# Performance work log

Hardware: AMD Instinct MI355X
Metric: run time of the kernel (lower is better)

The kernel has to match this reference:

```python
import jax, jax.numpy as jnp
import numpy as np

N, E = 10000, 80000
IN_C, HID, HEADS = 128, 256, 8
NEG_SLOPE = 0.2


def setup_inputs() -> dict:
    key = jax.random.key(0)
    ks = jax.random.split(key, 16)
    s = lambda k, shape, fan: jax.random.normal(k, shape, jnp.float32) * (1.0 / np.sqrt(fan))
    return {
        "x": jax.random.normal(ks[0], (N, IN_C), jnp.float32),
        "edge_index": jax.random.randint(ks[1], (2, E), 0, N, jnp.int64),
        "edge_weight": jax.random.uniform(ks[2], (E,), jnp.float32),
        # GATConv params
        "W_gat": s(ks[3], (IN_C, HEADS * HID), IN_C),
        "att_src": s(ks[4], (HEADS, HID), HID),
        "att_dst": s(ks[5], (HEADS, HID), HID),
        "b_gat": jnp.zeros((HEADS * HID,), jnp.float32),
        # SAGEConv params (lin_l on aggregated neighbors, lin_r on root)
        "W_sage_l": s(ks[6], (HEADS * HID, HID), HEADS * HID),
        "b_sage_l": jnp.zeros((HID,), jnp.float32),
        "W_sage_r": s(ks[7], (HEADS * HID, HID), HEADS * HID),
        # MLP head
        "W_lin1": s(ks[8], (HID, HID // 2), HID),
        "b_lin1": jnp.zeros((HID // 2,), jnp.float32),
        "W_lin2": s(ks[9], (HID // 2, 1), HID // 2),
        "b_lin2": jnp.zeros((1,), jnp.float32),
    }


def reference(x, edge_index, edge_weight, W_gat, att_src, att_dst, b_gat,
              W_sage_l, b_sage_l, W_sage_r, W_lin1, b_lin1, W_lin2, b_lin2):
    n = x.shape[0]
    src, dst = edge_index[0], edge_index[1]

    # ---- GATConv (edge_attr ignored since edge_dim=None in PyG) ----
    h = (x @ W_gat).reshape(n, HEADS, HID)            # [N,H,C]
    a_src = jnp.sum(h * att_src, axis=-1)             # [N,H]
    a_dst = jnp.sum(h * att_dst, axis=-1)             # [N,H]
    e = a_src[src] + a_dst[dst]                       # [E,H]
    e = jax.nn.leaky_relu(e, NEG_SLOPE)
    # segment softmax over edges sharing a destination node
    e_max = jax.ops.segment_max(e, dst, num_segments=n)   # [N,H]
    e_exp = jnp.exp(e - e_max[dst])                        # [E,H]
    denom = jax.ops.segment_sum(e_exp, dst, num_segments=n)
    alpha = e_exp / (denom[dst] + 1e-16)                   # [E,H]
    msg = h[src] * alpha[:, :, None]                       # [E,H,C]
    out1 = jax.ops.segment_sum(msg, dst, num_segments=n).reshape(n, HEADS * HID) + b_gat
    x1 = jax.nn.relu(out1)                                 # [N, H*C]; dropout is identity at inference

    # ---- SAGEConv (mean aggregation) ----
    deg = jax.ops.segment_sum(jnp.ones((src.shape[0],), x1.dtype), dst, num_segments=n)
    agg = jax.ops.segment_sum(x1[src], dst, num_segments=n) / jnp.maximum(deg, 1.0)[:, None]
    x2 = jax.nn.relu(agg @ W_sage_l + b_sage_l + x1 @ W_sage_r)  # [N, HID]

    # ---- MLP head ----
    hmid = jax.nn.relu(x2 @ W_lin1 + b_lin1)
    return hmid @ W_lin2 + b_lin2                           # [N,1]
```

## Files before the change

### kernel.cpp

```cpp
#include <hip/hip_runtime.h>
#include <math.h>

#define HEADS 8
#define HID 256
#define INC 128
#define GDIM 2048
#define NEG_SLOPE 0.2f
#define KSPLIT 2

typedef unsigned short ushort_t;
typedef short bf16x8 __attribute__((ext_vector_type(8)));
typedef ushort_t u16x8 __attribute__((ext_vector_type(8)));
typedef float f32x4 __attribute__((ext_vector_type(4)));

__device__ __forceinline__ ushort_t f2bf(float f) {
  union { float f; unsigned u; } v; v.f = f;
  unsigned r = (v.u + 0x7FFF + ((v.u >> 16) & 1)) >> 16;
  return (ushort_t)r;
}
__device__ __forceinline__ float bf2f(ushort_t u) {
  union { unsigned u; float f; } v; v.u = ((unsigned)u) << 16;
  return v.f;
}

__device__ __forceinline__ void gload_lds16(const ushort_t* g, ushort_t* l) {
  __builtin_amdgcn_global_load_lds(
      (const __attribute__((address_space(1))) unsigned int*)g,
      (__attribute__((address_space(3))) unsigned int*)l, 16, 0, 0);
}

__device__ __forceinline__ int src_chunk(int lane) {
  return ((lane & 3) - ((lane >> 3) & 3)) & 3;
}
__device__ __forceinline__ int rd_chunk(int lc, int kg) {
  return (kg + ((lc >> 1) & 3)) & 3;
}

__global__ __launch_bounds__(256) void zero_deg(int* __restrict__ deg, int n)
{
  int i = blockIdx.x * 256 + threadIdx.x;
  if (i < n) deg[i] = 0;
}

__global__ __launch_bounds__(256) void prep(
    const float* __restrict__ x, ushort_t* __restrict__ xb,
    const float* __restrict__ Wg, ushort_t* __restrict__ WgT,
    const float* __restrict__ Wl, const float* __restrict__ Wr, ushort_t* __restrict__ WsT,
    const int* __restrict__ ei, int* __restrict__ deg, int E,
    const float* __restrict__ att_s, const float* __restrict__ att_d, float* __restrict__ wt,
    int o1, int o2, int o3, int o4, int o5)
{
  __shared__ float tile[32][33];
  __shared__ float attl[256];
  int b = blockIdx.x, t = threadIdx.x;
  if (b < o1) {
    int i = b * 1024 + t * 4;
    float4 v = *(const float4*)(x + i);
    ushort_t o[4] = {f2bf(v.x), f2bf(v.y), f2bf(v.z), f2bf(v.w)};
    *(unsigned long long*)(xb + i) = *(unsigned long long*)o;
  } else if (b < o4) {
    const float* src; ushort_t* dst; int R, C, rowOff, bx, by;
    if (b < o2)      { int idx = b - o1; src = Wg; dst = WgT; R = INC;  C = GDIM; rowOff = 0;   bx = idx % (INC / 32);  by = idx / (INC / 32); }
    else if (b < o3) { int idx = b - o2; src = Wl; dst = WsT; R = GDIM; C = HID;  rowOff = 0;   bx = idx % (GDIM / 32); by = idx / (GDIM / 32); }
    else             { int idx = b - o3; src = Wr; dst = WsT; R = GDIM; C = HID;  rowOff = HID; bx = idx % (GDIM / 32); by = idx / (GDIM / 32); }
    int tx = t & 31, ty = t >> 5;
    int r0 = bx * 32, c0 = by * 32;
    #pragma unroll
    for (int i = 0; i < 32; i += 8)
      tile[ty + i][tx] = src[(size_t)(r0 + ty + i) * C + c0 + tx];
    __syncthreads();
    #pragma unroll
    for (int i = 0; i < 32; i += 8)
      dst[(size_t)(rowOff + c0 + ty + i) * R + r0 + tx] = f2bf(tile[tx][ty + i]);
  } else if (b < o5) {
    int e = (b - o4) * 256 + t;
    if (e < E) atomicAdd(&deg[ei[E + e]], 1);
  } else {
    int j = b - o5;
    int hd = j & 7;
    const float* att = (j < 8) ? att_s : att_d;
    if (t < 256) attl[t] = att[hd * 256 + t];
    __syncthreads();
    if (t < 128) {
      float acc = 0.f;
      #pragma unroll 8
      for (int c = 0; c < 256; ++c)
        acc += Wg[(size_t)t * GDIM + hd * 256 + c] * attl[c];
      wt[j * 128 + t] = acc;
    }
  }
}

__global__ __launch_bounds__(1024) void scan_deg(const int* __restrict__ deg, int* __restrict__ start,
                                                 int* __restrict__ cursor, int N)
{
  __shared__ int sums[1024];
  int t = threadIdx.x;
  int chunk = (N + 1023) / 1024;
  int s = 0;
  for (int i = 0; i < chunk; ++i) {
    int idx = t * chunk + i;
    if (idx < N) s += deg[idx];
  }
  sums[t] = s;
  __syncthreads();
  for (int off = 1; off < 1024; off <<= 1) {
    int v = (t >= off) ? sums[t - off] : 0;
    __syncthreads();
    sums[t] += v;
    __syncthreads();
  }
  int run = (t == 0) ? 0 : sums[t - 1];
  for (int i = 0; i < chunk; ++i) {
    int idx = t * chunk + i;
    if (idx < N) { start[idx] = run; cursor[idx] = run; run += deg[idx]; }
  }
}

__global__ __launch_bounds__(256) void fill_adots(
    const int* __restrict__ ei, int* __restrict__ cursor, int* __restrict__ srcs, int E, int nbFill,
    const ushort_t* __restrict__ xb, const float* __restrict__ wt,
    float* __restrict__ a_all, int N)
{
  int t = threadIdx.x;
  if (blockIdx.x < nbFill) {
    int e = blockIdx.x * 256 + t;
    if (e < E) {
      int n = ei[E + e];
      int p = atomicAdd(&cursor[n], 1);
      srcs[p] = ei[e];
    }
    return;
  }
  __shared__ float wts[16][132];
  __shared__ ushort_t xs[16 * 128];
  for (int i = t; i < 2048; i += 256) wts[i >> 7][i & 127] = wt[i];
  int b0 = (blockIdx.x - nbFill) * 16;
  {
    int row = t >> 4, off = (t & 15) * 8;
    int n = b0 + row; if (n >= N) n = N - 1;
    *(u16x8*)&xs[row * 128 + off] = *(const u16x8*)(xb + (size_t)n * 128 + off);
  }
  __syncthreads();
  int nl = t >> 4, j = t & 15;
  float acc = 0.f;
  #pragma unroll 8
  for (int k = 0; k < 128; ++k)
    acc += bf2f(xs[nl * 128 + k]) * wts[j][k];
  int n = b0 + nl;
  if (n < N) a_all[(size_t)n * 16 + j] = acc;
}

__global__ __launch_bounds__(256) void gat_aggregate(
    const ushort_t* __restrict__ xb, const float* __restrict__ a_all,
    const int* __restrict__ start, const int* __restrict__ deg,
    const int* __restrict__ srcs, ushort_t* __restrict__ aggb, int N)
{
  int n = blockIdx.x, t = threadIdx.x;
  __shared__ float adst[8];
  __shared__ float emax[8];
  __shared__ float esum[8];
  __shared__ float red[256];
  __shared__ float alpha_s[32][8];
  __shared__ int src_s[32];
  int cnt = deg[n];
  int base = start[n];
  if (t < 8) adst[t] = a_all[(size_t)n * 16 + 8 + t];
  __syncthreads();
  int hd = t & 7, lj = t >> 3;
  float m = -1e30f;
  for (int j = lj; j < cnt; j += 32) {
    int s = srcs[base + j];
    float v = a_all[(size_t)s * 16 + hd] + adst[hd];
    v = v > 0.f ? v : NEG_SLOPE * v;
    m = fmaxf(m, v);
  }
  red[t] = m;
  __syncthreads();
  #pragma unroll
  for (int off = 128; off >= 8; off >>= 1) {
    if (t < off) red[t] = fmaxf(red[t], red[t + off]);
    __syncthreads();
  }
  if (t < 8) emax[t] = red[t];
  __syncthreads();
  float ssum = 0.f;
  for (int j = lj; j < cnt; j += 32) {
    int s = srcs[base + j];
    float v = a_all[(size_t)s * 16 + hd] + adst[hd];
    v = v > 0.f ? v : NEG_SLOPE * v;
    ssum += expf(v - emax[hd]);
  }
  red[t] = ssum;
  __syncthreads();
  #pragma unroll
  for (int off = 128; off >= 8; off >>= 1) {
    if (t < off) red[t] += red[t + off];
    __syncthreads();
  }
  if (t < 8) esum[t] = red[t] + 1e-16f;
  __syncthreads();
  int d = t & 127, hg = t >> 7;
  float acc[4] = {0.f, 0.f, 0.f, 0.f};
  for (int j0 = 0; j0 < cnt; j0 += 32) {
    int j = j0 + lj;
    if (j < cnt) {
      int s = srcs[base + j];
      if (hd == 0) src_s[lj] = s;
      float v = a_all[(size_t)s * 16 + hd] + adst[hd];
      v = v > 0.f ? v : NEG_SLOPE * v;
      alpha_s[lj][hd] = expf(v - emax[hd]) / esum[hd];
    }
    __syncthreads();
    int lim = cnt - j0; if (lim > 32) lim = 32;
    for (int el = 0; el < lim; ++el) {
      float v = bf2f(xb[(size_t)src_s[el] * INC + d]);
      #pragma unroll
      for (int k = 0; k < 4; ++k) acc[k] += v * alpha_s[el][hg * 4 + k];
    }
    __syncthreads();
  }
  #pragma unroll
  for (int k = 0; k < 4; ++k)
    aggb[(size_t)n * 1024 + (hg * 4 + k) * INC + d] = f2bf(acc[k]);
}

__global__ __launch_bounds__(512) void gemm_gat(
    const ushort_t* __restrict__ A, const ushort_t* __restrict__ BT,
    const float* __restrict__ b_gat, ushort_t* __restrict__ x1, int M)
{
  __shared__ ushort_t As[2][128][32];
  __shared__ ushort_t Bs[2][256][32];
  int tid = threadIdx.x;
  int wave = tid >> 6, lane = tid & 63;
  int row0 = blockIdx.x * 128;
  int head = blockIdx.y;
  const ushort_t* Abase = A + head * INC;
  const ushort_t* Bbase = BT + (size_t)head * 256 * INC;
  int wr = (wave >> 2) * 64, wc = (wave & 3) * 64;
  int lc = lane & 15, kg = lane >> 4;
  int sc = src_chunk(lane), srow = lane >> 2;

  f32x4 acc[4][4] = {};

  #define STAGE_G(buf, kt)                                                        \
    {                                                                             \
      int ga = row0 + wave * 16 + srow; if (ga >= M) ga = M - 1;                  \
      gload_lds16(Abase + (size_t)ga * 1024 + (kt) + sc * 8, &As[buf][wave * 16][0]); \
      _Pragma("unroll")                                                           \
      for (int c = 0; c < 2; ++c) {                                               \
        int r = c * 128 + wave * 16 + srow;                                       \
        gload_lds16(Bbase + (size_t)r * INC + (kt) + sc * 8, &Bs[buf][c * 128 + wave * 16][0]); \
      }                                                                           \
    }

  #define COMPUTE_G(buf)                                                          \
    {                                                                             \
      bf16x8 af[4], bfr[4];                                                       \
      _Pragma("unroll")                                                           \
      for (int mi = 0; mi < 4; ++mi)                                              \
        af[mi] = *(const bf16x8*)&As[buf][wr + mi * 16 + lc][rd_chunk(lc, kg) * 8]; \
      _Pragma("unroll")                                                           \
      for (int ni = 0; ni < 4; ++ni)                                              \
        bfr[ni] = *(const bf16x8*)&Bs[buf][wc + ni * 16 + lc][rd_chunk(lc, kg) * 8]; \
      _Pragma("unroll")                                                           \
      for (int mi = 0; mi < 4; ++mi)                                              \
        _Pragma("unroll")                                                         \
        for (int ni = 0; ni < 4; ++ni)                                            \
          acc[mi][ni] = __builtin_amdgcn_mfma_f32_16x16x32_bf16(af[mi], bfr[ni], acc[mi][ni], 0, 0, 0); \
    }

  STAGE_G(0, 0);
  __syncthreads();
  int cur = 0;
  for (int kt = 32; kt < INC; kt += 32) {
    STAGE_G(cur ^ 1, kt);
    COMPUTE_G(cur);
    __syncthreads();
    cur ^= 1;
  }
  COMPUTE_G(cur);
  #undef STAGE_G
  #undef COMPUTE_G

  int gcol0 = head * 256;
  float bg[4];
  #pragma unroll
  for (int ni = 0; ni < 4; ++ni) bg[ni] = b_gat[gcol0 + wc + ni * 16 + lc];
  #pragma unroll
  for (int mi = 0; mi < 4; ++mi) {
    #pragma unroll
    for (int r = 0; r < 4; ++r) {
      int grow = row0 + wr + mi * 16 + kg * 4 + r;
      if (grow < M) {
        #pragma unroll
        for (int ni = 0; ni < 4; ++ni) {
          float v = acc[mi][ni][r] + bg[ni];
          x1[(size_t)grow * GDIM + gcol0 + wc + ni * 16 + lc] = f2bf(v > 0.f ? v : 0.f);
        }
      }
    }
  }
}

__global__ __launch_bounds__(512) void gemm_sage(
    const ushort_t* __restrict__ A, const ushort_t* __restrict__ BT,
    ushort_t* __restrict__ Cp, int M, int Nc, int K, int Klen)
{
  __shared__ ushort_t As[2][128][32];
  __shared__ ushort_t Bs[2][256][32];
  int tid = threadIdx.x;
  int wave = tid >> 6, lane = tid & 63;
  int row0 = blockIdx.x * 128, col0 = blockIdx.y * 256;
  int k0 = blockIdx.z * Klen;
  ushort_t* C = Cp + (size_t)blockIdx.z * M * Nc;
  int wr = (wave >> 2) * 64, wc = (wave & 3) * 64;
  int lc = lane & 15, kg = lane >> 4;
  int sc = src_chunk(lane), srow = lane >> 2;

  f32x4 acc[4][4] = {};

  #define STAGE_S(buf, kt)                                                        \
    {                                                                             \
      int ga = row0 + wave * 16 + srow; if (ga >= M) ga = M - 1;                  \
      gload_lds16(A + (size_t)ga * K + (kt) + sc * 8, &As[buf][wave * 16][0]);    \
      _Pragma("unroll")                                                           \
      for (int c = 0; c < 2; ++c) {                                               \
        int gb = col0 + c * 128 + wave * 16 + srow;                               \
        gload_lds16(BT + (size_t)gb * K + (kt) + sc * 8, &Bs[buf][c * 128 + wave * 16][0]); \
      }                                                                           \
    }

  #define COMPUTE_S(buf)                                                          \
    {                                                                             \
      bf16x8 af[4], bfr[4];                                                       \
      _Pragma("unroll")                                                           \
      for (int mi = 0; mi < 4; ++mi)                                              \
        af[mi] = *(const bf16x8*)&As[buf][wr + mi * 16 + lc][rd_chunk(lc, kg) * 8]; \
      _Pragma("unroll")                                                           \
      for (int ni = 0; ni < 4; ++ni)                                              \
        bfr[ni] = *(const bf16x8*)&Bs[buf][wc + ni * 16 + lc][rd_chunk(lc, kg) * 8]; \
      _Pragma("unroll")                                                           \
      for (int mi = 0; mi < 4; ++mi)                                              \
        _Pragma("unroll")                                                         \
        for (int ni = 0; ni < 4; ++ni)                                            \
          acc[mi][ni] = __builtin_amdgcn_mfma_f32_16x16x32_bf16(af[mi], bfr[ni], acc[mi][ni], 0, 0, 0); \
    }

  STAGE_S(0, k0);
  __syncthreads();
  int cur = 0;
  for (int kt = k0 + 32; kt < k0 + Klen; kt += 32) {
    STAGE_S(cur ^ 1, kt);
    COMPUTE_S(cur);
    __syncthreads();
    cur ^= 1;
  }
  COMPUTE_S(cur);
  #undef STAGE_S
  #undef COMPUTE_S

  #pragma unroll
  for (int mi = 0; mi < 4; ++mi) {
    #pragma unroll
    for (int r = 0; r < 4; ++r) {
      int grow = row0 + wr + mi * 16 + kg * 4 + r;
      if (grow < M) {
        #pragma unroll
        for (int ni = 0; ni < 4; ++ni)
          C[(size_t)grow * Nc + col0 + wc + ni * 16 + lc] = f2bf(acc[mi][ni][r]);
      }
    }
  }
}

__global__ __launch_bounds__(512) void sage_mlp(
    const ushort_t* __restrict__ yp, size_t ypstride,
    const int* __restrict__ start, const int* __restrict__ deg,
    const int* __restrict__ srcs, const float* __restrict__ b_l,
    const float* __restrict__ W1, const float* __restrict__ b1,
    const float* __restrict__ W2, const float* __restrict__ b2, float* __restrict__ out, int N)
{
  __shared__ float xs[16][256];
  __shared__ float wred[8][4];
  const ushort_t* yp0 = yp;
  const ushort_t* yp1 = yp + ypstride;
  int t = threadIdx.x;
  int wv = t >> 6, lane = t & 63;
  int b0 = blockIdx.x * 16;

  int half = lane >> 5;
  int col32 = lane & 31;
  #pragma unroll
  for (int i = 0; i < 2; ++i) {
    int nl = wv * 2 + i;
    int n = b0 + nl;
    float acc[8] = {0.f, 0.f, 0.f, 0.f, 0.f, 0.f, 0.f, 0.f};
    if (n < N) {
      int cnt = deg[n];
      int base = start[n];
      for (int j = 0; j < cnt; j += 2) {
        int jj = j + half;
        if (jj < cnt) {
          int s = srcs[base + jj];
          u16x8 v0 = *(const u16x8*)(yp0 + (size_t)s * 512 + col32 * 8);
          u16x8 v1 = *(const u16x8*)(yp1 + (size_t)s * 512 + col32 * 8);
          #pragma unroll
          for (int k = 0; k < 8; ++k) acc[k] += bf2f(v0[k]) + bf2f(v1[k]);
        }
      }
      #pragma unroll
      for (int k = 0; k < 8; ++k) acc[k] += __shfl_xor(acc[k], 32);
      if (half == 0) {
        float d = (float)cnt; if (d < 1.f) d = 1.f;
        u16x8 r0 = *(const u16x8*)(yp0 + (size_t)n * 512 + 256 + col32 * 8);
        u16x8 r1 = *(const u16x8*)(yp1 + (size_t)n * 512 + 256 + col32 * 8);
        #pragma unroll
        for (int k = 0; k < 8; ++k) {
          float v = acc[k] / d + bf2f(r0[k]) + bf2f(r1[k]) + b_l[col32 * 8 + k];
          xs[nl][col32 * 8 + k] = v > 0.f ? v : 0.f;
        }
      }
    } else if (half == 0) {
      #pragma unroll
      for (int k = 0; k < 8; ++k) xs[nl][col32 * 8 + k] = 0.f;
    }
  }
  __syncthreads();

  int c = t & 127, g = t >> 7;
  float acc[4];
  float bb = b1[c];
  #pragma unroll
  for (int nn = 0; nn < 4; ++nn) acc[nn] = bb;
  for (int k = 0; k < 256; ++k) {
    float w = W1[k * 128 + c];
    #pragma unroll
    for (int nn = 0; nn < 4; ++nn) acc[nn] += xs[g * 4 + nn][k] * w;
  }
  float w2 = W2[c];
  float p[4];
  #pragma unroll
  for (int nn = 0; nn < 4; ++nn) {
    float hm = acc[nn] > 0.f ? acc[nn] : 0.f;
    p[nn] = hm * w2;
  }
  #pragma unroll
  for (int off = 32; off >= 1; off >>= 1)
    #pragma unroll
    for (int nn = 0; nn < 4; ++nn) p[nn] += __shfl_down(p[nn], off);
  if (lane == 0) {
    #pragma unroll
    for (int nn = 0; nn < 4; ++nn) wred[wv][nn] = p[nn];
  }
  __syncthreads();
  if (t < 16) {
    int gg = t >> 2, nn = t & 3;
    int node = b0 + gg * 4 + nn;
    if (node < N)
      out[node] = wred[gg * 2][nn] + wred[gg * 2 + 1][nn] + b2[0];
  }
}

extern "C" void kernel_launch(void* const* d_in, const int* in_sizes, int n_in,
                              void* d_out, int out_size, void* d_ws, size_t ws_size,
                              hipStream_t stream)
{
  const float* x        = (const float*)d_in[0];
  const int*   ei       = (const int*)d_in[1];
  const float* W_gat    = (const float*)d_in[3];
  const float* att_src  = (const float*)d_in[4];
  const float* att_dst  = (const float*)d_in[5];
  const float* b_gat    = (const float*)d_in[6];
  const float* W_sage_l = (const float*)d_in[7];
  const float* b_sage_l = (const float*)d_in[8];
  const float* W_sage_r = (const float*)d_in[9];
  const float* W_lin1   = (const float*)d_in[10];
  const float* b_lin1   = (const float*)d_in[11];
  const float* W_lin2   = (const float*)d_in[12];
  const float* b_lin2   = (const float*)d_in[13];
  float* out = (float*)d_out;

  const int N = in_sizes[0] / INC;
  const int E = in_sizes[1] / 2;

  char* p = (char*)d_ws;
  ushort_t* x1b   = (ushort_t*)p;         p += (size_t)N * GDIM * 2;
  ushort_t* aggb  = (ushort_t*)p;         p += (size_t)N * 1024 * 2;
  ushort_t* ypart = (ushort_t*)p;         p += (size_t)KSPLIT * N * 512 * 2;
  ushort_t* xb    = (ushort_t*)p;         p += (size_t)N * INC * 2;
  ushort_t* WgatT = (ushort_t*)p;         p += (size_t)GDIM * INC * 2;
  ushort_t* WsT   = (ushort_t*)p;         p += (size_t)512 * GDIM * 2;
  float*    wt    = (float*)p;            p += (size_t)16 * 128 * 4;
  float*    a_all = (float*)p;            p += (size_t)N * 16 * 4;
  int*      deg   = (int*)p;              p += (size_t)N * 4;
  int*      start = (int*)p;              p += (size_t)N * 4;
  int*      cursor= (int*)p;              p += (size_t)N * 4;
  int*      srcs  = (int*)p;              p += (size_t)E * 4;

  zero_deg<<<(N + 255) / 256, 256, 0, stream>>>(deg, N);

  int nbX   = (N * INC + 1023) / 1024;
  int nbWg  = (INC / 32) * (GDIM / 32);
  int nbWs  = (GDIM / 32) * (HID / 32);
  int nbDeg = (E + 255) / 256;
  int o1 = nbX, o2 = o1 + nbWg, o3 = o2 + nbWs, o4 = o3 + nbWs, o5 = o4 + nbDeg;
  int nbTot = o5 + 16;
  prep<<<nbTot, 256, 0, stream>>>(x, xb, W_gat, WgatT, W_sage_l, W_sage_r, WsT,
                                  ei, deg, E, att_src, att_dst, wt, o1, o2, o3, o4, o5);

  scan_deg<<<1, 1024, 0, stream>>>(deg, start, cursor, N);

  { int nbFill = (E + 255) / 256;
    int nbDots = (N + 15) / 16;
    fill_adots<<<nbFill + nbDots, 256, 0, stream>>>(ei, cursor, srcs, E, nbFill,
                                                    xb, wt, a_all, N); }

  gat_aggregate<<<N, 256, 0, stream>>>(xb, a_all, start, deg, srcs, aggb, N);

  { dim3 grid((N + 127) / 128, HEADS);
    gemm_gat<<<grid, 512, 0, stream>>>(aggb, WgatT, b_gat, x1b, N); }

  { dim3 grid((N + 127) / 128, 512 / 256, KSPLIT);
    gemm_sage<<<grid, 512, 0, stream>>>(x1b, WsT, ypart, N, 512, GDIM, GDIM / KSPLIT); }

  sage_mlp<<<(N + 15) / 16, 512, 0, stream>>>(ypart, (size_t)N * 512, start, deg, srcs, b_sage_l,
                                              W_lin1, b_lin1, W_lin2, b_lin2, out, N);
}
```

Measured before the change: 162.2 us.

## Interleave split-K partials per row and prefetch neighbor indices in SAGE gather

The split-K partial outputs of the SAGE GEMM are now stored interleaved per node (row stride of 1024 bf16 holding both K-halves) instead of as two separate N×512 planes. Each gathered neighbor then reads its two partials from adjacent memory rather than from two distant buffers. The gather loop also prefetches the next source index before issuing the current loads, and the MLP k-loop gets an unroll-4 pragma. The GEMM's output writes become strided across a wider row, which may change its write efficiency.

```diff
diff --git a/kernel.cpp b/kernel.cpp
--- a/kernel.cpp
+++ b/kernel.cpp
@@ -305,7 +305,7 @@
 
 __global__ __launch_bounds__(512) void gemm_sage(
     const ushort_t* __restrict__ A, const ushort_t* __restrict__ BT,
-    ushort_t* __restrict__ Cp, int M, int Nc, int K, int Klen)
+    ushort_t* __restrict__ Cp, int M, int K, int Klen)
 {
   __shared__ ushort_t As[2][128][32];
   __shared__ ushort_t Bs[2][256][32];
@@ -313,7 +313,7 @@
   int wave = tid >> 6, lane = tid & 63;
   int row0 = blockIdx.x * 128, col0 = blockIdx.y * 256;
   int k0 = blockIdx.z * Klen;
-  ushort_t* C = Cp + (size_t)blockIdx.z * M * Nc;
+  ushort_t* C = Cp + (size_t)blockIdx.z * 512;
   int wr = (wave >> 2) * 64, wc = (wave & 3) * 64;
   int lc = lane & 15, kg = lane >> 4;
   int sc = src_chunk(lane), srow = lane >> 2;
@@ -368,14 +368,14 @@
       if (grow < M) {
         #pragma unroll
         for (int ni = 0; ni < 4; ++ni)
-          C[(size_t)grow * Nc + col0 + wc + ni * 16 + lc] = f2bf(acc[mi][ni][r]);
+          C[(size_t)grow * (KSPLIT * 512) + col0 + wc + ni * 16 + lc] = f2bf(acc[mi][ni][r]);
       }
     }
   }
 }
 
 __global__ __launch_bounds__(512) void sage_mlp(
-    const ushort_t* __restrict__ yp, size_t ypstride,
+    const ushort_t* __restrict__ yp,
     const int* __restrict__ start, const int* __restrict__ deg,
     const int* __restrict__ srcs, const float* __restrict__ b_l,
     const float* __restrict__ W1, const float* __restrict__ b1,
@@ -383,8 +383,6 @@
 {
   __shared__ float xs[16][256];
   __shared__ float wred[8][4];
-  const ushort_t* yp0 = yp;
-  const ushort_t* yp1 = yp + ypstride;
   int t = threadIdx.x;
   int wv = t >> 6, lane = t & 63;
   int b0 = blockIdx.x * 16;
@@ -399,22 +397,23 @@
     if (n < N) {
       int cnt = deg[n];
       int base = start[n];
-      for (int j = 0; j < cnt; j += 2) {
-        int jj = j + half;
-        if (jj < cnt) {
-          int s = srcs[base + jj];
-          u16x8 v0 = *(const u16x8*)(yp0 + (size_t)s * 512 + col32 * 8);
-          u16x8 v1 = *(const u16x8*)(yp1 + (size_t)s * 512 + col32 * 8);
-          #pragma unroll
-          for (int k = 0; k < 8; ++k) acc[k] += bf2f(v0[k]) + bf2f(v1[k]);
-        }
+      int jj = half;
+      int s_cur = (jj < cnt) ? srcs[base + jj] : 0;
+      while (jj < cnt) {
+        int jn = jj + 2;
+        int s_nxt = (jn < cnt) ? srcs[base + jn] : 0;
+        u16x8 v0 = *(const u16x8*)(yp + (size_t)s_cur * 1024 + col32 * 8);
+        u16x8 v1 = *(const u16x8*)(yp + (size_t)s_cur * 1024 + 512 + col32 * 8);
+        #pragma unroll
+        for (int k = 0; k < 8; ++k) acc[k] += bf2f(v0[k]) + bf2f(v1[k]);
+        jj = jn; s_cur = s_nxt;
       }
       #pragma unroll
       for (int k = 0; k < 8; ++k) acc[k] += __shfl_xor(acc[k], 32);
       if (half == 0) {
         float d = (float)cnt; if (d < 1.f) d = 1.f;
-        u16x8 r0 = *(const u16x8*)(yp0 + (size_t)n * 512 + 256 + col32 * 8);
-        u16x8 r1 = *(const u16x8*)(yp1 + (size_t)n * 512 + 256 + col32 * 8);
+        u16x8 r0 = *(const u16x8*)(yp + (size_t)n * 1024 + 256 + col32 * 8);
+        u16x8 r1 = *(const u16x8*)(yp + (size_t)n * 1024 + 512 + 256 + col32 * 8);
         #pragma unroll
         for (int k = 0; k < 8; ++k) {
           float v = acc[k] / d + bf2f(r0[k]) + bf2f(r1[k]) + b_l[col32 * 8 + k];
@@ -433,6 +432,7 @@
   float bb = b1[c];
   #pragma unroll
   for (int nn = 0; nn < 4; ++nn) acc[nn] = bb;
+  #pragma unroll 4
   for (int k = 0; k < 256; ++k) {
     float w = W1[k * 128 + c];
     #pragma unroll
@@ -522,8 +522,8 @@
     gemm_gat<<<grid, 512, 0, stream>>>(aggb, WgatT, b_gat, x1b, N); }
 
   { dim3 grid((N + 127) / 128, 512 / 256, KSPLIT);
-    gemm_sage<<<grid, 512, 0, stream>>>(x1b, WsT, ypart, N, 512, GDIM, GDIM / KSPLIT); }
-
-  sage_mlp<<<(N + 15) / 16, 512, 0, stream>>>(ypart, (size_t)N * 512, start, deg, srcs, b_sage_l,
+    gemm_sage<<<grid, 512, 0, stream>>>(x1b, WsT, ypart, N, GDIM, GDIM / KSPLIT); }
+
+  sage_mlp<<<(N + 15) / 16, 512, 0, stream>>>(ypart, start, deg, srcs, b_sage_l,
                                               W_lin1, b_lin1, W_lin2, b_lin2, out, N);
 }
```

New measurement: 163.0 us. Within noise of the previous version (+0.5%).
